# Optimization experiments

Measured on AMD Instinct MI355X. Metric: run time of the kernel, lower is better.

## Reference

```python
import jax, jax.numpy as jnp
import numpy as np

N = 50000          # num_nodes
E = 1600000        # num directed edges
IN_C = 128         # in_channels
OUT_C = 128        # out_channels
HEADS = 8
HFD = OUT_C // HEADS  # head_feat_dim = 16
NEG_SLOPE = 0.2


def setup_inputs() -> dict:
    key = jax.random.key(0)
    k1, k2, k3, k4, k5 = jax.random.split(key, 5)
    node_feats = jax.random.normal(k1, (N, IN_C), dtype=jnp.float32)
    edge_index = jax.random.randint(k2, (2, E), 0, N, dtype=jnp.int64)
    # parameters (xavier-ish scale, kept small so exp() stays in range)
    W = jax.random.normal(k3, (OUT_C, IN_C), dtype=jnp.float32) * (1.0 / np.sqrt(IN_C))
    a_left = jax.random.normal(k4, (HFD, HEADS), dtype=jnp.float32) * 0.1
    a_right = jax.random.normal(k5, (HFD, HEADS), dtype=jnp.float32) * 0.1
    bias = jnp.zeros((OUT_C,), dtype=jnp.float32)
    return {"node_feats": node_feats, "edge_index": edge_index,
            "W": W, "a_left": a_left, "a_right": a_right, "bias": bias}


def reference(node_feats, edge_index, W, a_left, a_right, bias):
    n = node_feats.shape[0]
    # embedding: Linear without bias, then split into heads -> [n, h, c]
    emb = (node_feats @ W.T).reshape(n, HEADS, HFD)
    # per-node attention logit halves: sum_c emb[n,h,c] * a[c,h] -> [n, h]
    left = jnp.einsum('nhc,ch->nh', emb, a_left)
    right = jnp.einsum('nhc,ch->nh', emb, a_right)
    src = edge_index[0]
    dst = edge_index[1]
    # edge logit: score(src, dst) uses a_left on src, a_right on dst
    e = left[src] + right[dst]                       # [E, h]
    e = jnp.where(e >= 0, e, NEG_SLOPE * e)          # leaky relu(0.2)
    w = jnp.exp(e)                                   # [E, h] (module uses raw exp)
    denom = jax.ops.segment_sum(w, dst, num_segments=n)  # [n, h]
    attn = w / denom[dst]                            # [E, h]
    msg = emb[src] * attn[:, :, None]                # [E, h, c]
    out = jax.ops.segment_sum(msg, dst, num_segments=n)  # [n, h, c]
    # concat heads + bias
    out = out.reshape(n, HEADS * HFD) + bias
    return out
```

## Files before the change

kernel.cpp:

```cpp
#include <hip/hip_runtime.h>
#include <hip/hip_bf16.h>

#define N_NODES 50000
#define N_EDGES 1600000
#define HEADS 8
#define HFD 16
#define CH 128

#define PART 128
#define NB 391
#define BCAP 5120
#define PA_T 512
#define PA_CHUNK 3200
#define PA_PER 7
#define PA_BLOCKS 500

typedef __bf16 bf16x8 __attribute__((ext_vector_type(8)));
typedef __bf16 bf16x4 __attribute__((ext_vector_type(4)));
typedef float f32x4 __attribute__((ext_vector_type(4)));

__device__ __forceinline__ float bf_lo(unsigned u) { return __uint_as_float(u << 16); }
__device__ __forceinline__ float bf_hi(unsigned u) { return __uint_as_float(u & 0xffff0000u); }

__global__ __launch_bounds__(256) void k_splitw(const float* __restrict__ W,
                                                const float* __restrict__ aL,
                                                const float* __restrict__ aR,
                                                __bf16* __restrict__ Whi,
                                                __bf16* __restrict__ Wlo,
                                                __bf16* __restrict__ Vhi,
                                                __bf16* __restrict__ Vlo,
                                                int* __restrict__ bucket_cnt) {
  int t = blockIdx.x * 256 + threadIdx.x;
  if (t < NB) bucket_cnt[t] = 0;
  if (t < CH * CH / 4) {
    f32x4 v = ((const f32x4*)W)[t];
    bf16x4 h, l;
#pragma unroll
    for (int i = 0; i < 4; ++i) {
      __bf16 hb = (__bf16)v[i];
      h[i] = hb;
      l[i] = (__bf16)(v[i] - (float)hb);
    }
    ((bf16x4*)Whi)[t] = h;
    ((bf16x4*)Wlo)[t] = l;
  }
  if (t < 16 * CH) {
    int j = t >> 7;
    int k = t & 127;
    int h = j & 7;
    const float* a = (j < 8) ? aL : aR;
    float v = 0.f;
#pragma unroll
    for (int c = 0; c < HFD; ++c) v += W[(h * HFD + c) * CH + k] * a[c * HEADS + h];
    __bf16 hb = (__bf16)v;
    Vhi[t] = hb;
    Vlo[t] = (__bf16)(v - (float)hb);
  }
}

__global__ __launch_bounds__(64) void k_emb(const float* __restrict__ X,
                                            const __bf16* __restrict__ Whi,
                                            const __bf16* __restrict__ Wlo,
                                            const __bf16* __restrict__ Vhi,
                                            const __bf16* __restrict__ Vlo,
                                            __bf16* __restrict__ embb,
                                            float* __restrict__ leftp,
                                            float* __restrict__ rightp) {
  int ntile = blockIdx.x;
  int lane = threadIdx.x;
  int c = lane & 15, quad = lane >> 4;
  const float* xp = X + (size_t)(ntile * 16 + c) * CH + quad * 8;
  bf16x8 xh[4], xl[4];
#pragma unroll
  for (int ks = 0; ks < 4; ++ks) {
    float4 x0 = *(const float4*)(xp + ks * 32);
    float4 x1 = *(const float4*)(xp + ks * 32 + 4);
    float xv[8] = {x0.x, x0.y, x0.z, x0.w, x1.x, x1.y, x1.z, x1.w};
#pragma unroll
    for (int j = 0; j < 8; ++j) {
      __bf16 hb = (__bf16)xv[j];
      xh[ks][j] = hb;
      xl[ks][j] = (__bf16)(xv[j] - (float)hb);
    }
  }
#pragma unroll
  for (int h = 0; h < HEADS; ++h) {
    const __bf16* wp = Whi + (size_t)(h * 16 + c) * CH + quad * 8;
    const __bf16* wlp = Wlo + (size_t)(h * 16 + c) * CH + quad * 8;
    f32x4 acc = {0.f, 0.f, 0.f, 0.f};
#pragma unroll
    for (int ks = 0; ks < 4; ++ks) {
      bf16x8 wh = *(const bf16x8*)(wp + ks * 32);
      bf16x8 wl = *(const bf16x8*)(wlp + ks * 32);
      acc = __builtin_amdgcn_mfma_f32_16x16x32_bf16(xl[ks], wh, acc, 0, 0, 0);
      acc = __builtin_amdgcn_mfma_f32_16x16x32_bf16(xh[ks], wl, acc, 0, 0, 0);
      acc = __builtin_amdgcn_mfma_f32_16x16x32_bf16(xh[ks], wh, acc, 0, 0, 0);
    }
#pragma unroll
    for (int r = 0; r < 4; ++r) {
      int node = ntile * 16 + quad * 4 + r;
      embb[(size_t)node * CH + h * HFD + c] = (__bf16)acc[r];
    }
  }
  {
    const __bf16* vp = Vhi + (size_t)c * CH + quad * 8;
    const __bf16* vlp = Vlo + (size_t)c * CH + quad * 8;
    f32x4 acc = {0.f, 0.f, 0.f, 0.f};
#pragma unroll
    for (int ks = 0; ks < 4; ++ks) {
      bf16x8 vh = *(const bf16x8*)(vp + ks * 32);
      bf16x8 vl = *(const bf16x8*)(vlp + ks * 32);
      acc = __builtin_amdgcn_mfma_f32_16x16x32_bf16(xl[ks], vh, acc, 0, 0, 0);
      acc = __builtin_amdgcn_mfma_f32_16x16x32_bf16(xh[ks], vl, acc, 0, 0, 0);
      acc = __builtin_amdgcn_mfma_f32_16x16x32_bf16(xh[ks], vh, acc, 0, 0, 0);
    }
#pragma unroll
    for (int r = 0; r < 4; ++r) {
      int node = ntile * 16 + quad * 4 + r;
      if (c < 8) leftp[node * HEADS + c] = acc[r];
      else rightp[node * HEADS + (c - 8)] = acc[r];
    }
  }
}

__global__ __launch_bounds__(PA_T) void k_bucket(const int* __restrict__ ei,
                                                 int* __restrict__ bucket_cnt,
                                                 unsigned* __restrict__ ebuf) {
  __shared__ unsigned sp[PA_CHUNK];
  __shared__ int hist[NB];
  __shared__ int lcur[NB];
  __shared__ int wbase[NB];
  __shared__ int scn[PA_T];
  int t = threadIdx.x;
  int base = blockIdx.x * PA_CHUNK;
  for (int i = t; i < NB; i += PA_T) hist[i] = 0;
  __syncthreads();
  unsigned pk[PA_PER];
#pragma unroll
  for (int i = 0; i < PA_PER; ++i) {
    int e = t + i * PA_T;
    pk[i] = 0xffffffffu;
    if (e < PA_CHUNK) {
      int src = ei[base + e];
      int dst = ei[N_EDGES + base + e];
      pk[i] = ((unsigned)(dst >> 7) << 23) | ((unsigned)(dst & 127) << 16) |
              (unsigned)src;
      atomicAdd(&hist[dst >> 7], 1);
    }
  }
  __syncthreads();
  scn[t] = (t < NB) ? hist[t] : 0;
  __syncthreads();
  int val = scn[t];
  for (int d = 1; d < PA_T; d <<= 1) {
    int o = (t >= d) ? scn[t - d] : 0;
    __syncthreads();
    val += o;
    scn[t] = val;
    __syncthreads();
  }
  if (t < NB) {
    int hv = hist[t];
    int lstart = val - hv;
    lcur[t] = lstart;
    int prior = hv ? atomicAdd(&bucket_cnt[t], hv) : 0;
    wbase[t] = t * BCAP + prior - lstart;
  }
  __syncthreads();
#pragma unroll
  for (int i = 0; i < PA_PER; ++i) {
    if (pk[i] != 0xffffffffu) {
      int b = pk[i] >> 23;
      int pos = atomicAdd(&lcur[b], 1);
      sp[pos] = pk[i];
    }
  }
  __syncthreads();
  for (int i = t; i < PA_CHUNK; i += PA_T) {
    unsigned p = sp[i];
    int b = p >> 23;
    int slot = wbase[b] + i;
    if (slot < (b + 1) * BCAP) ebuf[slot] = p;
  }
}

__global__ __launch_bounds__(512) void k_aggr(const int* __restrict__ bucket_cnt,
                                              const unsigned* __restrict__ ebuf,
                                              const __bf16* __restrict__ embb,
                                              const float* __restrict__ leftp,
                                              const float* __restrict__ rightp,
                                              const float* __restrict__ bias,
                                              float* __restrict__ out) {
  __shared__ unsigned short su[BCAP];
  __shared__ int hist[PART];
  __shared__ int pfx[PART];
  __shared__ int cur[PART];
  int b = blockIdx.x >> 1;
  int half = blockIdx.x & 1;
  int t = threadIdx.x;
  int cnt = bucket_cnt[b];
  if (cnt > BCAP) cnt = BCAP;
  int ebase = b * BCAP;
  if (t < PART) hist[t] = 0;
  __syncthreads();
  for (int e = t; e < cnt; e += 512)
    atomicAdd(&hist[(ebuf[ebase + e] >> 16) & 127], 1);
  __syncthreads();
  if (t < PART) pfx[t] = hist[t];
  __syncthreads();
  for (int d = 1; d < PART; d <<= 1) {
    int v = 0;
    if (t < PART) { v = pfx[t]; if (t >= d) v += pfx[t - d]; }
    __syncthreads();
    if (t < PART) pfx[t] = v;
    __syncthreads();
  }
  if (t < PART) {
    int excl = pfx[t] - hist[t];
    pfx[t] = excl;
    cur[t] = excl;
  }
  __syncthreads();
  for (int e = t; e < cnt; e += 512) {
    unsigned p = ebuf[ebase + e];
    int pos = atomicAdd(&cur[(p >> 16) & 127], 1);
    su[pos] = (unsigned short)(p & 0xffffu);
  }
  __syncthreads();

  int wv = t >> 6;
  int lane = t & 63;
  int g = lane >> 4;
  int m = lane & 15;
  int h = m >> 1;
#pragma unroll
  for (int k = 0; k < 8; ++k) {
    int dl = half * 64 + wv * 8 + k;
    int dst = b * PART + dl;
    bool valid = dst < N_NODES;
    int beg = pfx[dl];
    int cd = hist[dl];
    float r = valid ? rightp[dst * HEADS + h] : 0.f;
    float acc[8] = {0.f, 0.f, 0.f, 0.f, 0.f, 0.f, 0.f, 0.f};
    float dsum = 0.f;
    for (int e0 = 0; e0 < cd; e0 += 8) {
      int i0 = e0 + g, i1 = e0 + 4 + g;
      bool a0 = i0 < cd, a1 = i1 < cd;
      int s0 = su[beg + (a0 ? i0 : 0)];
      int s1 = su[beg + (a1 ? i1 : 0)];
      uint4 u0 = ((const uint4*)(embb + (size_t)s0 * CH))[m];
      uint4 u1 = ((const uint4*)(embb + (size_t)s1 * CH))[m];
      float l0 = leftp[s0 * HEADS + h];
      float l1 = leftp[s1 * HEADS + h];
      float x0 = l0 + r;
      x0 = (x0 >= 0.f) ? x0 : 0.2f * x0;
      float w0 = a0 ? __expf(x0) : 0.f;
      float x1 = l1 + r;
      x1 = (x1 >= 0.f) ? x1 : 0.2f * x1;
      float w1 = a1 ? __expf(x1) : 0.f;
      dsum += w0 + w1;
      acc[0] += w0 * bf_lo(u0.x) + w1 * bf_lo(u1.x);
      acc[1] += w0 * bf_hi(u0.x) + w1 * bf_hi(u1.x);
      acc[2] += w0 * bf_lo(u0.y) + w1 * bf_lo(u1.y);
      acc[3] += w0 * bf_hi(u0.y) + w1 * bf_hi(u1.y);
      acc[4] += w0 * bf_lo(u0.z) + w1 * bf_lo(u1.z);
      acc[5] += w0 * bf_hi(u0.z) + w1 * bf_hi(u1.z);
      acc[6] += w0 * bf_lo(u0.w) + w1 * bf_lo(u1.w);
      acc[7] += w0 * bf_hi(u0.w) + w1 * bf_hi(u1.w);
    }
#pragma unroll
    for (int mask = 16; mask <= 32; mask <<= 1) {
      dsum += __shfl_xor(dsum, mask);
#pragma unroll
      for (int j = 0; j < 8; ++j) acc[j] += __shfl_xor(acc[j], mask);
    }
    if (g == 0 && valid) {
      float inv = (dsum > 0.f) ? 1.0f / dsum : 0.f;
      float4 b0 = ((const float4*)bias)[2 * m];
      float4 b1 = ((const float4*)bias)[2 * m + 1];
      float4 o0 = {acc[0] * inv + b0.x, acc[1] * inv + b0.y,
                   acc[2] * inv + b0.z, acc[3] * inv + b0.w};
      float4 o1 = {acc[4] * inv + b1.x, acc[5] * inv + b1.y,
                   acc[6] * inv + b1.z, acc[7] * inv + b1.w};
      ((float4*)(out + (size_t)dst * CH))[2 * m] = o0;
      ((float4*)(out + (size_t)dst * CH))[2 * m + 1] = o1;
    }
  }
}

extern "C" void kernel_launch(void* const* d_in, const int* in_sizes, int n_in,
                              void* d_out, int out_size, void* d_ws, size_t ws_size,
                              hipStream_t stream) {
  const float* X = (const float*)d_in[0];
  const int* ei = (const int*)d_in[1];
  const float* W = (const float*)d_in[2];
  const float* al = (const float*)d_in[3];
  const float* ar = (const float*)d_in[4];
  const float* bias = (const float*)d_in[5];
  float* out = (float*)d_out;

  unsigned* ebuf = (unsigned*)d_ws;
  __bf16* embb = (__bf16*)(ebuf + (size_t)NB * BCAP);
  __bf16* Whi = embb + (size_t)N_NODES * CH;
  __bf16* Wlo = Whi + CH * CH;
  __bf16* Vhi = Wlo + CH * CH;
  __bf16* Vlo = Vhi + 16 * CH;
  float* leftp = (float*)(Vlo + 16 * CH);
  float* rightp = leftp + (size_t)N_NODES * HEADS;
  int* bucket_cnt = (int*)(rightp + (size_t)N_NODES * HEADS);

  k_splitw<<<16, 256, 0, stream>>>(W, al, ar, Whi, Wlo, Vhi, Vlo, bucket_cnt);
  k_bucket<<<PA_BLOCKS, PA_T, 0, stream>>>(ei, bucket_cnt, ebuf);
  k_emb<<<N_NODES / 16, 64, 0, stream>>>(X, Whi, Wlo, Vhi, Vlo, embb, leftp, rightp);
  k_aggr<<<NB * 2, 512, 0, stream>>>(bucket_cnt, ebuf, embb, leftp, rightp, bias, out);
}
```

Measured before the change: 211.4 us.

## Fuse bucketing with embedding, precompute fp16 edge weights, split aggregation by channel quarter

```diff
diff --git a/kernel.cpp b/kernel.cpp
--- a/kernel.cpp
+++ b/kernel.cpp
@@ -1,5 +1,6 @@
 #include <hip/hip_runtime.h>
 #include <hip/hip_bf16.h>
+#include <hip/hip_fp16.h>
 
 #define N_NODES 50000
 #define N_EDGES 1600000
@@ -10,10 +11,12 @@
 #define PART 128
 #define NB 391
 #define BCAP 5120
+#define NSLOT (NB * BCAP)
 #define PA_T 512
 #define PA_CHUNK 3200
 #define PA_PER 7
 #define PA_BLOCKS 500
+#define EMB_BLOCKS 391
 
 typedef __bf16 bf16x8 __attribute__((ext_vector_type(8)));
 typedef __bf16 bf16x4 __attribute__((ext_vector_type(4)));
@@ -22,14 +25,14 @@
 __device__ __forceinline__ float bf_lo(unsigned u) { return __uint_as_float(u << 16); }
 __device__ __forceinline__ float bf_hi(unsigned u) { return __uint_as_float(u & 0xffff0000u); }
 
-__global__ __launch_bounds__(256) void k_splitw(const float* __restrict__ W,
-                                                const float* __restrict__ aL,
-                                                const float* __restrict__ aR,
-                                                __bf16* __restrict__ Whi,
-                                                __bf16* __restrict__ Wlo,
-                                                __bf16* __restrict__ Vhi,
-                                                __bf16* __restrict__ Vlo,
-                                                int* __restrict__ bucket_cnt) {
+__global__ __launch_bounds__(256) void k_prep(const float* __restrict__ W,
+                                              const float* __restrict__ aL,
+                                              const float* __restrict__ aR,
+                                              __bf16* __restrict__ Whi,
+                                              __bf16* __restrict__ Wlo,
+                                              __bf16* __restrict__ Vhi,
+                                              __bf16* __restrict__ Vlo,
+                                              int* __restrict__ bucket_cnt) {
   int t = blockIdx.x * 256 + threadIdx.x;
   if (t < NB) bucket_cnt[t] = 0;
   if (t < CH * CH / 4) {
@@ -58,153 +61,153 @@
   }
 }
 
-__global__ __launch_bounds__(64) void k_emb(const float* __restrict__ X,
-                                            const __bf16* __restrict__ Whi,
-                                            const __bf16* __restrict__ Wlo,
-                                            const __bf16* __restrict__ Vhi,
-                                            const __bf16* __restrict__ Vlo,
-                                            __bf16* __restrict__ embb,
-                                            float* __restrict__ leftp,
-                                            float* __restrict__ rightp) {
-  int ntile = blockIdx.x;
-  int lane = threadIdx.x;
-  int c = lane & 15, quad = lane >> 4;
-  const float* xp = X + (size_t)(ntile * 16 + c) * CH + quad * 8;
-  bf16x8 xh[4], xl[4];
-#pragma unroll
-  for (int ks = 0; ks < 4; ++ks) {
-    float4 x0 = *(const float4*)(xp + ks * 32);
-    float4 x1 = *(const float4*)(xp + ks * 32 + 4);
-    float xv[8] = {x0.x, x0.y, x0.z, x0.w, x1.x, x1.y, x1.z, x1.w};
-#pragma unroll
-    for (int j = 0; j < 8; ++j) {
-      __bf16 hb = (__bf16)xv[j];
-      xh[ks][j] = hb;
-      xl[ks][j] = (__bf16)(xv[j] - (float)hb);
-    }
-  }
-#pragma unroll
-  for (int h = 0; h < HEADS; ++h) {
-    const __bf16* wp = Whi + (size_t)(h * 16 + c) * CH + quad * 8;
-    const __bf16* wlp = Wlo + (size_t)(h * 16 + c) * CH + quad * 8;
-    f32x4 acc = {0.f, 0.f, 0.f, 0.f};
-#pragma unroll
-    for (int ks = 0; ks < 4; ++ks) {
-      bf16x8 wh = *(const bf16x8*)(wp + ks * 32);
-      bf16x8 wl = *(const bf16x8*)(wlp + ks * 32);
-      acc = __builtin_amdgcn_mfma_f32_16x16x32_bf16(xl[ks], wh, acc, 0, 0, 0);
-      acc = __builtin_amdgcn_mfma_f32_16x16x32_bf16(xh[ks], wl, acc, 0, 0, 0);
-      acc = __builtin_amdgcn_mfma_f32_16x16x32_bf16(xh[ks], wh, acc, 0, 0, 0);
-    }
-#pragma unroll
-    for (int r = 0; r < 4; ++r) {
-      int node = ntile * 16 + quad * 4 + r;
-      embb[(size_t)node * CH + h * HFD + c] = (__bf16)acc[r];
-    }
-  }
-  {
-    const __bf16* vp = Vhi + (size_t)c * CH + quad * 8;
-    const __bf16* vlp = Vlo + (size_t)c * CH + quad * 8;
-    f32x4 acc = {0.f, 0.f, 0.f, 0.f};
-#pragma unroll
-    for (int ks = 0; ks < 4; ++ks) {
-      bf16x8 vh = *(const bf16x8*)(vp + ks * 32);
-      bf16x8 vl = *(const bf16x8*)(vlp + ks * 32);
-      acc = __builtin_amdgcn_mfma_f32_16x16x32_bf16(xl[ks], vh, acc, 0, 0, 0);
-      acc = __builtin_amdgcn_mfma_f32_16x16x32_bf16(xh[ks], vl, acc, 0, 0, 0);
-      acc = __builtin_amdgcn_mfma_f32_16x16x32_bf16(xh[ks], vh, acc, 0, 0, 0);
-    }
-#pragma unroll
-    for (int r = 0; r < 4; ++r) {
-      int node = ntile * 16 + quad * 4 + r;
-      if (c < 8) leftp[node * HEADS + c] = acc[r];
-      else rightp[node * HEADS + (c - 8)] = acc[r];
-    }
-  }
-}
-
-__global__ __launch_bounds__(PA_T) void k_bucket(const int* __restrict__ ei,
-                                                 int* __restrict__ bucket_cnt,
-                                                 unsigned* __restrict__ ebuf) {
+__global__ __launch_bounds__(512) void k_fused(const int* __restrict__ ei,
+                                               int* __restrict__ bucket_cnt,
+                                               unsigned* __restrict__ ebuf,
+                                               const float* __restrict__ X,
+                                               const __bf16* __restrict__ Whi,
+                                               const __bf16* __restrict__ Wlo,
+                                               const __bf16* __restrict__ Vhi,
+                                               const __bf16* __restrict__ Vlo,
+                                               __bf16* __restrict__ embb,
+                                               float* __restrict__ leftp,
+                                               float* __restrict__ rightp) {
   __shared__ unsigned sp[PA_CHUNK];
   __shared__ int hist[NB];
   __shared__ int lcur[NB];
   __shared__ int wbase[NB];
   __shared__ int scn[PA_T];
   int t = threadIdx.x;
-  int base = blockIdx.x * PA_CHUNK;
-  for (int i = t; i < NB; i += PA_T) hist[i] = 0;
-  __syncthreads();
-  unsigned pk[PA_PER];
-#pragma unroll
-  for (int i = 0; i < PA_PER; ++i) {
-    int e = t + i * PA_T;
-    pk[i] = 0xffffffffu;
-    if (e < PA_CHUNK) {
-      int src = ei[base + e];
-      int dst = ei[N_EDGES + base + e];
-      pk[i] = ((unsigned)(dst >> 7) << 23) | ((unsigned)(dst & 127) << 16) |
-              (unsigned)src;
-      atomicAdd(&hist[dst >> 7], 1);
-    }
-  }
-  __syncthreads();
-  scn[t] = (t < NB) ? hist[t] : 0;
-  __syncthreads();
-  int val = scn[t];
-  for (int d = 1; d < PA_T; d <<= 1) {
-    int o = (t >= d) ? scn[t - d] : 0;
-    __syncthreads();
-    val += o;
-    scn[t] = val;
-    __syncthreads();
-  }
-  if (t < NB) {
-    int hv = hist[t];
-    int lstart = val - hv;
-    lcur[t] = lstart;
-    int prior = hv ? atomicAdd(&bucket_cnt[t], hv) : 0;
-    wbase[t] = t * BCAP + prior - lstart;
-  }
-  __syncthreads();
-#pragma unroll
-  for (int i = 0; i < PA_PER; ++i) {
-    if (pk[i] != 0xffffffffu) {
-      int b = pk[i] >> 23;
-      int pos = atomicAdd(&lcur[b], 1);
-      sp[pos] = pk[i];
-    }
-  }
-  __syncthreads();
-  for (int i = t; i < PA_CHUNK; i += PA_T) {
-    unsigned p = sp[i];
-    int b = p >> 23;
-    int slot = wbase[b] + i;
-    if (slot < (b + 1) * BCAP) ebuf[slot] = p;
-  }
-}
-
-__global__ __launch_bounds__(512) void k_aggr(const int* __restrict__ bucket_cnt,
+  if (blockIdx.x < PA_BLOCKS) {
+    int base = blockIdx.x * PA_CHUNK;
+    for (int i = t; i < NB; i += PA_T) hist[i] = 0;
+    __syncthreads();
+    unsigned pk[PA_PER];
+#pragma unroll
+    for (int i = 0; i < PA_PER; ++i) {
+      int e = t + i * PA_T;
+      pk[i] = 0xffffffffu;
+      if (e < PA_CHUNK) {
+        int src = ei[base + e];
+        int dst = ei[N_EDGES + base + e];
+        pk[i] = ((unsigned)(dst >> 7) << 23) | ((unsigned)(dst & 127) << 16) |
+                (unsigned)src;
+        atomicAdd(&hist[dst >> 7], 1);
+      }
+    }
+    __syncthreads();
+    scn[t] = (t < NB) ? hist[t] : 0;
+    __syncthreads();
+    int val = scn[t];
+    for (int d = 1; d < PA_T; d <<= 1) {
+      int o = (t >= d) ? scn[t - d] : 0;
+      __syncthreads();
+      val += o;
+      scn[t] = val;
+      __syncthreads();
+    }
+    if (t < NB) {
+      int hv = hist[t];
+      int lstart = val - hv;
+      lcur[t] = lstart;
+      int prior = hv ? atomicAdd(&bucket_cnt[t], hv) : 0;
+      wbase[t] = t * BCAP + prior - lstart;
+    }
+    __syncthreads();
+#pragma unroll
+    for (int i = 0; i < PA_PER; ++i) {
+      if (pk[i] != 0xffffffffu) {
+        int b = pk[i] >> 23;
+        int pos = atomicAdd(&lcur[b], 1);
+        sp[pos] = pk[i];
+      }
+    }
+    __syncthreads();
+    for (int i = t; i < PA_CHUNK; i += PA_T) {
+      unsigned p = sp[i];
+      int b = p >> 23;
+      int slot = wbase[b] + i;
+      if (slot < (b + 1) * BCAP) ebuf[slot] = p;
+    }
+  } else {
+    int tile = (blockIdx.x - PA_BLOCKS) * 8 + (t >> 6);
+    if (tile >= N_NODES / 16) return;
+    int lane = t & 63;
+    int c = lane & 15, quad = lane >> 4;
+    const float* xp = X + (size_t)(tile * 16 + c) * CH + quad * 8;
+    bf16x8 xh[4], xl[4];
+#pragma unroll
+    for (int ks = 0; ks < 4; ++ks) {
+      float4 x0 = *(const float4*)(xp + ks * 32);
+      float4 x1 = *(const float4*)(xp + ks * 32 + 4);
+      float xv[8] = {x0.x, x0.y, x0.z, x0.w, x1.x, x1.y, x1.z, x1.w};
+#pragma unroll
+      for (int j = 0; j < 8; ++j) {
+        __bf16 hb = (__bf16)xv[j];
+        xh[ks][j] = hb;
+        xl[ks][j] = (__bf16)(xv[j] - (float)hb);
+      }
+    }
+#pragma unroll
+    for (int h = 0; h < HEADS; ++h) {
+      const __bf16* wp = Whi + (size_t)(h * 16 + c) * CH + quad * 8;
+      const __bf16* wlp = Wlo + (size_t)(h * 16 + c) * CH + quad * 8;
+      f32x4 acc = {0.f, 0.f, 0.f, 0.f};
+#pragma unroll
+      for (int ks = 0; ks < 4; ++ks) {
+        bf16x8 wh = *(const bf16x8*)(wp + ks * 32);
+        bf16x8 wl = *(const bf16x8*)(wlp + ks * 32);
+        acc = __builtin_amdgcn_mfma_f32_16x16x32_bf16(xl[ks], wh, acc, 0, 0, 0);
+        acc = __builtin_amdgcn_mfma_f32_16x16x32_bf16(xh[ks], wl, acc, 0, 0, 0);
+        acc = __builtin_amdgcn_mfma_f32_16x16x32_bf16(xh[ks], wh, acc, 0, 0, 0);
+      }
+#pragma unroll
+      for (int r = 0; r < 4; ++r) {
+        int node = tile * 16 + quad * 4 + r;
+        embb[(size_t)node * CH + h * HFD + c] = (__bf16)acc[r];
+      }
+    }
+    {
+      const __bf16* vp = Vhi + (size_t)c * CH + quad * 8;
+      const __bf16* vlp = Vlo + (size_t)c * CH + quad * 8;
+      f32x4 acc = {0.f, 0.f, 0.f, 0.f};
+#pragma unroll
+      for (int ks = 0; ks < 4; ++ks) {
+        bf16x8 vh = *(const bf16x8*)(vp + ks * 32);
+        bf16x8 vl = *(const bf16x8*)(vlp + ks * 32);
+        acc = __builtin_amdgcn_mfma_f32_16x16x32_bf16(xl[ks], vh, acc, 0, 0, 0);
+        acc = __builtin_amdgcn_mfma_f32_16x16x32_bf16(xh[ks], vl, acc, 0, 0, 0);
+        acc = __builtin_amdgcn_mfma_f32_16x16x32_bf16(xh[ks], vh, acc, 0, 0, 0);
+      }
+#pragma unroll
+      for (int r = 0; r < 4; ++r) {
+        int node = tile * 16 + quad * 4 + r;
+        if (c < 8) leftp[node * HEADS + c] = acc[r];
+        else rightp[node * HEADS + (c - 8)] = acc[r];
+      }
+    }
+  }
+}
+
+__global__ __launch_bounds__(512) void k_csrw(const int* __restrict__ bucket_cnt,
                                               const unsigned* __restrict__ ebuf,
-                                              const __bf16* __restrict__ embb,
                                               const float* __restrict__ leftp,
                                               const float* __restrict__ rightp,
-                                              const float* __restrict__ bias,
-                                              float* __restrict__ out) {
-  __shared__ unsigned short su[BCAP];
+                                              int* __restrict__ rowptr,
+                                              int* __restrict__ deg,
+                                              unsigned short* __restrict__ su,
+                                              unsigned* __restrict__ wpl) {
   __shared__ int hist[PART];
   __shared__ int pfx[PART];
   __shared__ int cur[PART];
-  int b = blockIdx.x >> 1;
-  int half = blockIdx.x & 1;
-  int t = threadIdx.x;
+  int b = blockIdx.x, t = threadIdx.x;
   int cnt = bucket_cnt[b];
   if (cnt > BCAP) cnt = BCAP;
   int ebase = b * BCAP;
   if (t < PART) hist[t] = 0;
   __syncthreads();
   for (int e = t; e < cnt; e += 512)
-    atomicAdd(&hist[(ebuf[ebase + e] >> 16) & 127], 1);
+    atomicAdd(&hist[(__builtin_nontemporal_load(&ebuf[ebase + e]) >> 16) & 127], 1);
   __syncthreads();
   if (t < PART) pfx[t] = hist[t];
   __syncthreads();
@@ -217,47 +220,85 @@
   }
   if (t < PART) {
     int excl = pfx[t] - hist[t];
-    pfx[t] = excl;
     cur[t] = excl;
+    int dst = b * PART + t;
+    if (dst < N_NODES) {
+      rowptr[dst] = ebase + excl;
+      deg[dst] = hist[t];
+    }
   }
   __syncthreads();
   for (int e = t; e < cnt; e += 512) {
-    unsigned p = ebuf[ebase + e];
-    int pos = atomicAdd(&cur[(p >> 16) & 127], 1);
-    su[pos] = (unsigned short)(p & 0xffffu);
-  }
-  __syncthreads();
-
-  int wv = t >> 6;
-  int lane = t & 63;
-  int g = lane >> 4;
-  int m = lane & 15;
-  int h = m >> 1;
+    unsigned p = __builtin_nontemporal_load(&ebuf[ebase + e]);
+    int dl = (p >> 16) & 127;
+    int src = p & 0xffffu;
+    int pos = ebase + atomicAdd(&cur[dl], 1);
+    su[pos] = (unsigned short)src;
+    int dst = b * PART + dl;
+    const float4* lp = (const float4*)(leftp + src * HEADS);
+    const float4* rp = (const float4*)(rightp + dst * HEADS);
+    float4 l0 = lp[0], l1 = lp[1];
+    float4 r0 = rp[0], r1 = rp[1];
+    float w[8];
+    float xs[8] = {l0.x + r0.x, l0.y + r0.y, l0.z + r0.z, l0.w + r0.w,
+                   l1.x + r1.x, l1.y + r1.y, l1.z + r1.z, l1.w + r1.w};
+#pragma unroll
+    for (int h = 0; h < 8; ++h) {
+      float x = xs[h];
+      x = (x >= 0.f) ? x : 0.2f * x;
+      w[h] = __expf(x);
+    }
+#pragma unroll
+    for (int q = 0; q < 4; ++q) {
+      __half2 h2 = __floats2half2_rn(w[2 * q], w[2 * q + 1]);
+      wpl[(size_t)q * NSLOT + pos] = *(const unsigned*)&h2;
+    }
+  }
+}
+
+__global__ __launch_bounds__(512) void k_aggr(const int* __restrict__ rowptr,
+                                              const int* __restrict__ deg,
+                                              const unsigned short* __restrict__ su,
+                                              const unsigned* __restrict__ wpl,
+                                              const __bf16* __restrict__ embb,
+                                              const float* __restrict__ bias,
+                                              float* __restrict__ out) {
+  int i = blockIdx.x;
+  int q = i & 3;
+  int hb = i >> 2;
+  int b = hb >> 1, half = hb & 1;
+  int t = threadIdx.x, wv = t >> 6, lane = t & 63;
+  int g = lane >> 2;
+  int m = lane & 3;
+  int hsel = m >> 1;
+  const unsigned* wq = wpl + (size_t)q * NSLOT;
+  const __bf16* embq = embb + q * 32;
+  float4 b0 = ((const float4*)bias)[q * 8 + m * 2];
+  float4 b1 = ((const float4*)bias)[q * 8 + m * 2 + 1];
 #pragma unroll
   for (int k = 0; k < 8; ++k) {
     int dl = half * 64 + wv * 8 + k;
     int dst = b * PART + dl;
     bool valid = dst < N_NODES;
-    int beg = pfx[dl];
-    int cd = hist[dl];
-    float r = valid ? rightp[dst * HEADS + h] : 0.f;
+    int beg = __builtin_amdgcn_readfirstlane(valid ? rowptr[dst] : 0);
+    int cd = __builtin_amdgcn_readfirstlane(valid ? deg[dst] : 0);
     float acc[8] = {0.f, 0.f, 0.f, 0.f, 0.f, 0.f, 0.f, 0.f};
     float dsum = 0.f;
-    for (int e0 = 0; e0 < cd; e0 += 8) {
-      int i0 = e0 + g, i1 = e0 + 4 + g;
+    for (int e0 = 0; e0 < cd; e0 += 32) {
+      int i0 = e0 + g, i1 = e0 + 16 + g;
       bool a0 = i0 < cd, a1 = i1 < cd;
-      int s0 = su[beg + (a0 ? i0 : 0)];
-      int s1 = su[beg + (a1 ? i1 : 0)];
-      uint4 u0 = ((const uint4*)(embb + (size_t)s0 * CH))[m];
-      uint4 u1 = ((const uint4*)(embb + (size_t)s1 * CH))[m];
-      float l0 = leftp[s0 * HEADS + h];
-      float l1 = leftp[s1 * HEADS + h];
-      float x0 = l0 + r;
-      x0 = (x0 >= 0.f) ? x0 : 0.2f * x0;
-      float w0 = a0 ? __expf(x0) : 0.f;
-      float x1 = l1 + r;
-      x1 = (x1 >= 0.f) ? x1 : 0.2f * x1;
-      float w1 = a1 ? __expf(x1) : 0.f;
+      int sl0 = beg + (a0 ? i0 : 0);
+      int sl1 = beg + (a1 ? i1 : 0);
+      int s0 = __builtin_nontemporal_load(&su[sl0]);
+      int s1 = __builtin_nontemporal_load(&su[sl1]);
+      unsigned wv0 = __builtin_nontemporal_load(&wq[sl0]);
+      unsigned wv1 = __builtin_nontemporal_load(&wq[sl1]);
+      uint4 u0 = ((const uint4*)(embq + (size_t)s0 * CH))[m];
+      uint4 u1 = ((const uint4*)(embq + (size_t)s1 * CH))[m];
+      float2 wf0 = __half22float2(*(const __half2*)&wv0);
+      float2 wf1 = __half22float2(*(const __half2*)&wv1);
+      float w0 = a0 ? (hsel ? wf0.y : wf0.x) : 0.f;
+      float w1 = a1 ? (hsel ? wf1.y : wf1.x) : 0.f;
       dsum += w0 + w1;
       acc[0] += w0 * bf_lo(u0.x) + w1 * bf_lo(u1.x);
       acc[1] += w0 * bf_hi(u0.x) + w1 * bf_hi(u1.x);
@@ -269,21 +310,20 @@
       acc[7] += w0 * bf_hi(u0.w) + w1 * bf_hi(u1.w);
     }
 #pragma unroll
-    for (int mask = 16; mask <= 32; mask <<= 1) {
+    for (int mask = 4; mask <= 32; mask <<= 1) {
       dsum += __shfl_xor(dsum, mask);
 #pragma unroll
       for (int j = 0; j < 8; ++j) acc[j] += __shfl_xor(acc[j], mask);
     }
     if (g == 0 && valid) {
       float inv = (dsum > 0.f) ? 1.0f / dsum : 0.f;
-      float4 b0 = ((const float4*)bias)[2 * m];
-      float4 b1 = ((const float4*)bias)[2 * m + 1];
-      float4 o0 = {acc[0] * inv + b0.x, acc[1] * inv + b0.y,
-                   acc[2] * inv + b0.z, acc[3] * inv + b0.w};
-      float4 o1 = {acc[4] * inv + b1.x, acc[5] * inv + b1.y,
-                   acc[6] * inv + b1.z, acc[7] * inv + b1.w};
-      ((float4*)(out + (size_t)dst * CH))[2 * m] = o0;
-      ((float4*)(out + (size_t)dst * CH))[2 * m + 1] = o1;
+      f32x4 o0 = {acc[0] * inv + b0.x, acc[1] * inv + b0.y,
+                  acc[2] * inv + b0.z, acc[3] * inv + b0.w};
+      f32x4 o1 = {acc[4] * inv + b1.x, acc[5] * inv + b1.y,
+                  acc[6] * inv + b1.z, acc[7] * inv + b1.w};
+      f32x4* op = (f32x4*)(out + (size_t)dst * CH + q * 32);
+      __builtin_nontemporal_store(o0, &op[m * 2]);
+      __builtin_nontemporal_store(o1, &op[m * 2 + 1]);
     }
   }
 }
@@ -300,17 +340,22 @@
   float* out = (float*)d_out;
 
   unsigned* ebuf = (unsigned*)d_ws;
-  __bf16* embb = (__bf16*)(ebuf + (size_t)NB * BCAP);
-  __bf16* Whi = embb + (size_t)N_NODES * CH;
+  unsigned* wpl = ebuf + NSLOT;
+  __bf16* embb = (__bf16*)(wpl + 4 * (size_t)NSLOT);
+  unsigned short* su = (unsigned short*)(embb + (size_t)N_NODES * CH);
+  int* rowptr = (int*)(su + NSLOT);
+  int* deg = rowptr + N_NODES;
+  int* bucket_cnt = deg + N_NODES;
+  __bf16* Whi = (__bf16*)(bucket_cnt + 400);
   __bf16* Wlo = Whi + CH * CH;
   __bf16* Vhi = Wlo + CH * CH;
   __bf16* Vlo = Vhi + 16 * CH;
   float* leftp = (float*)(Vlo + 16 * CH);
   float* rightp = leftp + (size_t)N_NODES * HEADS;
-  int* bucket_cnt = (int*)(rightp + (size_t)N_NODES * HEADS);
-
-  k_splitw<<<16, 256, 0, stream>>>(W, al, ar, Whi, Wlo, Vhi, Vlo, bucket_cnt);
-  k_bucket<<<PA_BLOCKS, PA_T, 0, stream>>>(ei, bucket_cnt, ebuf);
-  k_emb<<<N_NODES / 16, 64, 0, stream>>>(X, Whi, Wlo, Vhi, Vlo, embb, leftp, rightp);
-  k_aggr<<<NB * 2, 512, 0, stream>>>(bucket_cnt, ebuf, embb, leftp, rightp, bias, out);
-}
+
+  k_prep<<<16, 256, 0, stream>>>(W, al, ar, Whi, Wlo, Vhi, Vlo, bucket_cnt);
+  k_fused<<<PA_BLOCKS + EMB_BLOCKS, 512, 0, stream>>>(ei, bucket_cnt, ebuf, X, Whi,
+                                                      Wlo, Vhi, Vlo, embb, leftp, rightp);
+  k_csrw<<<NB, 512, 0, stream>>>(bucket_cnt, ebuf, leftp, rightp, rowptr, deg, su, wpl);
+  k_aggr<<<NB * 2 * 4, 512, 0, stream>>>(rowptr, deg, su, wpl, embb, bias, out);
+}
```

Result: slower. 325.1 us (+53.8%).
